# Kernel optimization log

Hardware: AMD Instinct MI355X
Metric: run time of the kernel (lower is better)

Reference implementation:

```python
import jax, jax.numpy as jnp
import numpy as np
import math

N = 20000      # nodes
E = 150000     # edges
IN = 256       # in_dim
HID = 256      # n_hid / out_dim
T = 4          # num_types
R = 8          # num_relations
H = 8          # n_heads
DK = HID // H  # d_k = 32
L = 2          # n_layers
MAXLEN = 240   # RTE max_len


def _rte_table():
    # fixed sinusoid table from RelTemporalEncoding (requires_grad=False in torch)
    pos = np.arange(MAXLEN, dtype=np.float64)[:, None]
    div = np.exp(np.arange(0, HID, 2, dtype=np.float64) * -(math.log(10000.0) / HID))
    emb = np.zeros((MAXLEN, HID), dtype=np.float64)
    emb[:, 0::2] = np.sin(pos * div) / math.sqrt(HID)
    emb[:, 1::2] = np.cos(pos * div) / math.sqrt(HID)
    return jnp.asarray(emb, dtype=jnp.float32)


def setup_inputs() -> dict:
    key = jax.random.key(0)
    ks = jax.random.split(key, 20)
    node_feature = jax.random.normal(ks[0], (N, IN), jnp.float32)
    node_type = jax.random.randint(ks[1], (N,), 0, T)
    edge_index = jax.random.randint(ks[2], (2, E), 0, N)
    edge_type = jax.random.randint(ks[3], (E,), 0, R)
    edge_time = jax.random.randint(ks[4], (E,), 0, MAXLEN)

    s_in = 1.0 / math.sqrt(IN)
    s_h = 1.0 / math.sqrt(HID)
    s_g = math.sqrt(2.0 / (DK + DK))  # glorot for relation mats

    adapt_W = jax.random.normal(ks[5], (T, IN, HID), jnp.float32) * s_in
    adapt_b = jnp.zeros((T, HID), jnp.float32)
    k_W = jax.random.normal(ks[6], (L, T, HID, HID), jnp.float32) * s_h
    k_b = jnp.zeros((L, T, HID), jnp.float32)
    q_W = jax.random.normal(ks[7], (L, T, HID, HID), jnp.float32) * s_h
    q_b = jnp.zeros((L, T, HID), jnp.float32)
    v_W = jax.random.normal(ks[8], (L, T, HID, HID), jnp.float32) * s_h
    v_b = jnp.zeros((L, T, HID), jnp.float32)
    a_W = jax.random.normal(ks[9], (L, T, HID, HID), jnp.float32) * s_h
    a_b = jnp.zeros((L, T, HID), jnp.float32)
    rel_pri = jnp.ones((L, R, H), jnp.float32)
    rel_att = jax.random.normal(ks[10], (L, R, H, DK, DK), jnp.float32) * s_g
    rel_msg = jax.random.normal(ks[11], (L, R, H, DK, DK), jnp.float32) * s_g
    skip = jnp.ones((L, T), jnp.float32)
    rte_W = jax.random.normal(ks[12], (L, HID, HID), jnp.float32) * s_h
    rte_b = jnp.zeros((L, HID), jnp.float32)
    rte_emb = _rte_table()

    return dict(node_feature=node_feature, node_type=node_type, edge_time=edge_time,
                edge_index=edge_index, edge_type=edge_type,
                adapt_W=adapt_W, adapt_b=adapt_b, k_W=k_W, k_b=k_b, q_W=q_W, q_b=q_b,
                v_W=v_W, v_b=v_b, a_W=a_W, a_b=a_b, rel_pri=rel_pri, rel_att=rel_att,
                rel_msg=rel_msg, skip=skip, rte_W=rte_W, rte_b=rte_b, rte_emb=rte_emb)


def _typed_linear(x, W, b, types):
    # x: [M, din]; W: [T, din, dout]; per-row type-selected linear (T dense GEMMs + select)
    out = jnp.zeros((x.shape[0], W.shape[-1]), x.dtype)
    for t in range(T):
        out = jnp.where((types == t)[:, None], x @ W[t] + b[t], out)
    return out


def _hgt_forward(node_feature, node_type, edge_time, edge_index, edge_type,
                 adapt_W, adapt_b, k_W, k_b, q_W, q_b, v_W, v_b, a_W, a_b,
                 rel_pri, rel_att, rel_msg, skip, rte_W, rte_b, rte_emb):
    # adapt: per-type tanh(Linear) (dropout is identity at p=0)
    x = jnp.tanh(_typed_linear(node_feature, adapt_W, adapt_b, node_type))
    src, tgt = edge_index[0], edge_index[1]   # j (source), i (target)
    st, tt = node_type[src], node_type[tgt]
    sqrt_dk = math.sqrt(DK)
    att = None
    rte = rte_emb[edge_time]                  # [E, HID]
    for l in range(L):
        x_j = x[src] + (rte @ rte_W[l] + rte_b[l])   # RTE added to source repr
        x_i = x[tgt]
        q = _typed_linear(x_i, q_W[l], q_b[l], tt).reshape(E, H, DK)
        k = _typed_linear(x_j, k_W[l], k_b[l], st).reshape(E, H, DK)
        v = _typed_linear(x_j, v_W[l], v_b[l], st).reshape(E, H, DK)
        att_e = jnp.zeros((E, H), x.dtype)
        msg = jnp.zeros((E, H, DK), x.dtype)
        for r in range(R):
            kr = jnp.einsum('ehd,hdk->ehk', k, rel_att[l, r])
            vr = jnp.einsum('ehd,hdk->ehk', v, rel_msg[l, r])
            a = (q * kr).sum(-1) * rel_pri[l, r] / sqrt_dk
            m = edge_type == r
            att_e = jnp.where(m[:, None], a, att_e)
            msg = jnp.where(m[:, None, None], vr, msg)
        # segment softmax over target node ids
        amax = jax.ops.segment_max(att_e, tgt, num_segments=N)
        ex = jnp.exp(att_e - amax[tgt])
        denom = jax.ops.segment_sum(ex, tgt, num_segments=N)
        alpha = ex / denom[tgt]                       # [E, H]
        agg = jax.ops.segment_sum(msg * alpha[:, :, None], tgt, num_segments=N)
        agg = jax.nn.gelu(agg.reshape(N, HID), approximate=False)
        trans = _typed_linear(agg, a_W[l], a_b[l], node_type)
        sk = jax.nn.sigmoid(skip[l])[node_type][:, None]
        x = trans * sk + x * (1.0 - sk)               # no LayerNorm (use_norm=False)
        att = alpha
    return att, x


def reference(node_feature, node_type, edge_time, edge_index, edge_type,
              adapt_W, adapt_b, k_W, k_b, q_W, q_b, v_W, v_b, a_W, a_b,
              rel_pri, rel_att, rel_msg, skip, rte_W, rte_b, rte_emb):
    return _hgt_forward(node_feature, node_type, edge_time, edge_index, edge_type,
                        adapt_W, adapt_b, k_W, k_b, q_W, q_b, v_W, v_b, a_W, a_b,
                        rel_pri, rel_att, rel_msg, skip, rte_W, rte_b, rte_emb)
```

## Files before the change

### kernel.cpp

```cpp
#include <hip/hip_runtime.h>
#include <hip/hip_fp16.h>

#define NN    20000
#define NE    150000
#define HD    256
#define NT    4
#define NR    8
#define NH    8
#define DKq   32
#define NL    2
#define MAXL  240
#define HBLK  256
#define SCB   ((NN + 255)/256)
#define TMAX  632
#define FOLDN 79
#define FOLDC 15
#define INV_SQRT_DK 0.17677669529663687f

typedef _Float16 f16x4 __attribute__((ext_vector_type(4)));
typedef float    f32x4v __attribute__((ext_vector_type(4)));

__global__ __launch_bounds__(256) void k_nhist(const int* __restrict__ ntype, int* __restrict__ nhist)
{
    __shared__ int h[NT];
    const int tid = threadIdx.x, b = blockIdx.x;
    if (tid < NT) h[tid] = 0;
    __syncthreads();
    const int cn = (NN + HBLK-1)/HBLK;
    const int nEnd = min((b+1)*cn, NN);
    for (int i = b*cn + tid; i < nEnd; i += 256) atomicAdd(&h[ntype[i]], 1);
    __syncthreads();
    if (tid < NT) nhist[b*NT + tid] = h[tid];
}
__global__ void k_nscan(const int* __restrict__ nhist, int* __restrict__ noff, int* __restrict__ nbase,
                        int* __restrict__ tlist, int* __restrict__ tcount)
{
    __shared__ int tot[NT];
    const int tid = threadIdx.x;
    if (tid < NT){
        int s = 0;
        for (int b = 0; b < HBLK; b++) s += nhist[b*NT + tid];
        tot[tid] = s;
    }
    __syncthreads();
    if (tid == 0){ noff[0]=0; for (int t=0;t<NT;t++) noff[t+1]=noff[t]+tot[t]; }
    if (tid < NT){
        int base = 0; for (int t=0;t<tid;t++) base += tot[t];
        int run = 0;
        for (int b=0;b<HBLK;b++){ nbase[b*NT+tid] = base + run; run += nhist[b*NT+tid]; }
    }
    __syncthreads();
    if (tid == 0){
        int c = 0;
        for (int t = 0; t < NT; t++){
            const int ntile = (tot[t] + 31) >> 5;
            for (int rt = 0; rt < ntile; rt++) tlist[c++] = (t << 20) | rt;
        }
        *tcount = c;
    }
}
__global__ __launch_bounds__(256) void k_nscatter(const int* __restrict__ ntype,
    const int* __restrict__ nbase, int* __restrict__ nbucket)
{
    __shared__ int cur[NT];
    const int tid = threadIdx.x, b = blockIdx.x;
    if (tid < NT) cur[tid] = nbase[b*NT + tid];
    __syncthreads();
    const int cn = (NN + HBLK-1)/HBLK;
    const int nEnd = min((b+1)*cn, NN);
    for (int i = b*cn + tid; i < nEnd; i += 256)
        nbucket[atomicAdd(&cur[ntype[i]], 1)] = i;
}

__global__ void k_zero_bins(int* __restrict__ cnt){
    int i = blockIdx.x*256 + threadIdx.x;
    if (i < NN) cnt[i] = 0;
}
__global__ void k_csr_hist(const int* __restrict__ ei, int* __restrict__ cnt){
    int e = blockIdx.x*256 + threadIdx.x;
    if (e >= NE) return;
    atomicAdd(&cnt[ei[NE+e]], 1);
}
__global__ __launch_bounds__(256) void k_scan1(const int* __restrict__ cnt,
    int* __restrict__ tgt_off, int* __restrict__ bsum)
{
    __shared__ int sh[256];
    const int t = threadIdx.x, b = blockIdx.x;
    const int i = b*256 + t;
    const int v = (i < NN) ? cnt[i] : 0;
    sh[t] = v;
    __syncthreads();
    #pragma unroll
    for (int d = 1; d < 256; d <<= 1){
        const int u = (t >= d) ? sh[t-d] : 0;
        __syncthreads();
        sh[t] += u;
        __syncthreads();
    }
    if (i < NN) tgt_off[i] = sh[t] - v;
    if (t == 255) bsum[b] = sh[255];
}
__global__ __launch_bounds__(128) void k_scan2(const int* __restrict__ bsum,
    int* __restrict__ bbase, int* __restrict__ tgt_off)
{
    __shared__ int sh[128];
    const int t = threadIdx.x;
    const int v = (t < SCB) ? bsum[t] : 0;
    sh[t] = v;
    __syncthreads();
    #pragma unroll
    for (int d = 1; d < 128; d <<= 1){
        const int u = (t >= d) ? sh[t-d] : 0;
        __syncthreads();
        sh[t] += u;
        __syncthreads();
    }
    if (t < SCB) bbase[t] = sh[t] - v;
    if (t == 0) tgt_off[NN] = NE;
}
__global__ __launch_bounds__(256) void k_scan3(int* __restrict__ tgt_off,
    const int* __restrict__ bbase, int* __restrict__ binCur)
{
    const int i = blockIdx.x*256 + threadIdx.x;
    if (i >= NN) return;
    const int o = tgt_off[i] + bbase[blockIdx.x];
    tgt_off[i] = o;
    binCur[i] = o;
}
__global__ void k_csr_scatter(const int* __restrict__ ei, const int* __restrict__ etype,
    const int* __restrict__ etime, const int* __restrict__ ntype,
    int* __restrict__ binCur, int* __restrict__ src_s, int* __restrict__ combo_s,
    int* __restrict__ eid_s, int* __restrict__ tgt_s)
{
    int e = blockIdx.x*256 + threadIdx.x;
    if (e >= NE) return;
    const int tgt = ei[NE+e], r = etype[e], src = ei[e];
    const int pos = atomicAdd(&binCur[tgt], 1);
    src_s[pos] = src;
    combo_s[pos] = (etime[e]*NT + ntype[src]) | (r << 12);
    eid_s[pos] = e;
    tgt_s[pos] = tgt;
}

__global__ __launch_bounds__(256) void k_w2f16_big(
    const float* __restrict__ adaptW, const float* __restrict__ qW, const float* __restrict__ kW,
    const float* __restrict__ vW, const float* __restrict__ aW, _Float16* __restrict__ out)
{
    const int y = blockIdx.y;
    const float* src; int m;
    if (y < 4){ src = adaptW; m = y; }
    else if (y < 12){ src = qW; m = y-4; }
    else if (y < 20){ src = kW; m = y-12; }
    else if (y < 28){ src = vW; m = y-20; }
    else { src = aW; m = y-28; }
    const float* ip = src + (size_t)m*65536;
    _Float16* op = out + (size_t)y*65536;
    const int tid4 = blockIdx.x*256 + threadIdx.x;
    const int k4 = tid4 >> 8, c = tid4 & 255;
    f16x4 hv;
    #pragma unroll
    for (int j = 0; j < 4; j++)
        hv[j] = (_Float16)ip[(size_t)(((k4*4 + j) << 8) + c)];
    *reinterpret_cast<f16x4*>(&op[(size_t)tid4 * 4]) = hv;
}
__global__ __launch_bounds__(256) void k_w2f16_rel(
    const float* __restrict__ attW, const float* __restrict__ msgW, _Float16* __restrict__ out)
{
    const int y = blockIdx.y;
    const float* ip = (y < 128) ? (attW + (size_t)y*1024) : (msgW + (size_t)(y-128)*1024);
    _Float16* op = out + (size_t)y*1024;
    const int tid4 = threadIdx.x;
    const int k4 = tid4 >> 5, c = tid4 & 31;
    f16x4 hv;
    #pragma unroll
    for (int j = 0; j < 4; j++)
        hv[j] = (_Float16)ip[(size_t)(((k4*4 + j) << 5) + c)];
    *reinterpret_cast<f16x4*>(&op[(size_t)tid4 * 4]) = hv;
}

__global__ __launch_bounds__(256) void k_typed_mfma(
    const float* __restrict__ inF, const _Float16* __restrict__ inH,
    const _Float16* __restrict__ W0, const _Float16* __restrict__ W1, const _Float16* __restrict__ W2,
    const float* __restrict__ b0, const float* __restrict__ b1, const float* __restrict__ b2,
    void* __restrict__ o0, void* __restrict__ o1, void* __restrict__ o2,
    const int* __restrict__ nbucket, const int* __restrict__ noff,
    const int* __restrict__ tlist, const int* __restrict__ tcount,
    int nsel, int mode, int out_half_mask, const float* __restrict__ skipv, const float* __restrict__ xold)
{
    if ((int)blockIdx.x >= *tcount) return;
    const int ent = tlist[blockIdx.x];
    const int t = ent >> 20, rowTile = ent & 0xFFFFF;
    const int start = noff[t], cnt = noff[t+1] - start;

    const int tid = threadIdx.x;
    const int w = tid >> 6, lane = tid & 63;
    const int lrow = lane & 15, lgrp = lane >> 4;

    __shared__ _Float16 Al[32][260];
    __shared__ int nid[32];

    if (tid < 32){
        const int gr = rowTile*32 + tid;
        nid[tid] = (gr < cnt) ? nbucket[start + gr] : -1;
    }
    __syncthreads();

    {
        const int r = tid >> 3;
        const int arow = nid[r];
        if (inH){
            const _Float16* ap = (arow >= 0) ? (inH + (size_t)arow*HD) : nullptr;
            #pragma unroll
            for (int j = 0; j < 8; j++){
                const int f4 = (tid & 7) + j*8;
                f16x4 hv = {0,0,0,0};
                if (ap) hv = *reinterpret_cast<const f16x4*>(ap + f4*4);
                *reinterpret_cast<f16x4*>(&Al[r][f4*4]) = hv;
            }
        } else {
            const float* ap = (arow >= 0) ? (inF + (size_t)arow*HD) : nullptr;
            #pragma unroll
            for (int j = 0; j < 8; j++){
                const int f4 = (tid & 7) + j*8;
                float4 v = make_float4(0.f,0.f,0.f,0.f);
                if (ap) v = *reinterpret_cast<const float4*>(ap + f4*4);
                f16x4 hv;
                hv[0]=(_Float16)v.x; hv[1]=(_Float16)v.y; hv[2]=(_Float16)v.z; hv[3]=(_Float16)v.w;
                *reinterpret_cast<f16x4*>(&Al[r][f4*4]) = hv;
            }
        }
    }
    __syncthreads();

    float sk = 0.f;
    if (mode == 2) sk = 1.f/(1.f + __expf(-skipv[t]));

    auto proc = [&](const _Float16* Wb, const float* bb, void* out, int oh){
        const _Float16* W = Wb + (size_t)t*HD*HD;
        const float* bias = bb + (size_t)t*HD;
        f32x4v acc[4][2];
        #pragma unroll
        for (int cs = 0; cs < 4; cs++){
            acc[cs][0] = (f32x4v){0.f,0.f,0.f,0.f};
            acc[cs][1] = (f32x4v){0.f,0.f,0.f,0.f};
        }
        #pragma unroll 4
        for (int kc = 0; kc < 16; kc++){
            f16x4 bf[4];
            #pragma unroll
            for (int cs = 0; cs < 4; cs++)
                bf[cs] = *reinterpret_cast<const f16x4*>(
                    &W[(size_t)((kc*4 + lgrp)*HD + w*64 + cs*16 + lrow)*4]);
            const f16x4 af0 = *reinterpret_cast<const f16x4*>(&Al[lrow][kc*16 + lgrp*4]);
            const f16x4 af1 = *reinterpret_cast<const f16x4*>(&Al[16 + lrow][kc*16 + lgrp*4]);
            #pragma unroll
            for (int cs = 0; cs < 4; cs++){
                acc[cs][0] = __builtin_amdgcn_mfma_f32_16x16x16f16(af0, bf[cs], acc[cs][0], 0,0,0);
                acc[cs][1] = __builtin_amdgcn_mfma_f32_16x16x16f16(af1, bf[cs], acc[cs][1], 0,0,0);
            }
        }
        #pragma unroll
        for (int cs = 0; cs < 4; cs++){
            const int col = w*64 + cs*16 + lrow;
            const float bcol = bias[col];
            #pragma unroll
            for (int rt = 0; rt < 2; rt++){
                #pragma unroll
                for (int i = 0; i < 4; i++){
                    const int lr = rt*16 + lgrp*4 + i;
                    const int gr = rowTile*32 + lr;
                    if (gr >= cnt) continue;
                    const int node = nid[lr];
                    float v = acc[cs][rt][i] + bcol;
                    if (mode == 1) v = tanhf(v);
                    else if (mode == 2){
                        const float xo = xold[(size_t)node*HD + col];
                        v = v*sk + xo*(1.f - sk);
                    }
                    if (oh) ((_Float16*)out)[(size_t)node*HD + col] = (_Float16)v;
                    else    ((float*)out)[(size_t)node*HD + col] = v;
                }
            }
        }
    };

    proc(W0, b0, o0, out_half_mask & 1);
    if (nsel > 1){
        proc(W1, b1, o1, (out_half_mask >> 1) & 1);
        proc(W2, b2, o2, (out_half_mask >> 2) & 1);
    }
}

__global__ __launch_bounds__(256) void k_row_gemm(
    const float* __restrict__ A, const float* __restrict__ W, const float* __restrict__ bias,
    float* __restrict__ C)
{
    const int row = blockIdx.x, d = threadIdx.x;
    __shared__ float ar[HD];
    ar[d] = A[(size_t)row*HD + d];
    __syncthreads();
    float acc = bias[d];
    #pragma unroll 8
    for (int k=0;k<HD;k++) acc = fmaf(ar[k], W[(size_t)k*HD + d], acc);
    C[(size_t)row*HD + d] = acc;
}
__global__ __launch_bounds__(256) void k_row_gemm2(
    const float* __restrict__ A, const float* __restrict__ kWb, const float* __restrict__ vWb,
    _Float16* __restrict__ Kc, _Float16* __restrict__ Vc)
{
    const int row = blockIdx.x, ty = blockIdx.y, d = threadIdx.x;
    const float* W = ((blockIdx.z == 0) ? kWb : vWb) + (size_t)ty*HD*HD;
    _Float16* C = (blockIdx.z == 0) ? Kc : Vc;
    __shared__ float ar[HD];
    ar[d] = A[(size_t)row*HD + d];
    __syncthreads();
    float acc = 0.f;
    #pragma unroll 8
    for (int k=0;k<HD;k++) acc = fmaf(ar[k], W[(size_t)k*HD + d], acc);
    C[(size_t)row*(NT*HD) + ty*HD + d] = (_Float16)acc;
}

__global__ __launch_bounds__(256) void k_fold_mfma(
    const _Float16* __restrict__ INn, const _Float16* __restrict__ INc,
    const _Float16* __restrict__ MATF,
    _Float16* __restrict__ OUTn, _Float16* __restrict__ OUTc)
{
    const int r = blockIdx.y;
    const bool isC = (int)blockIdx.x >= FOLDN;
    const int bx0 = isC ? (int)blockIdx.x - FOLDN : (int)blockIdx.x;
    const _Float16* IN = isC ? INc : INn;
    _Float16* OUT = isC ? OUTc : OUTn;
    const int M = isC ? (MAXL*NT) : NN;
    const int bstride = (isC ? FOLDC : FOLDN) * 4;

    const int lane = threadIdx.x & 63, w = threadIdx.x >> 6;
    const int lrow = lane & 15, lgrp = lane >> 4;
    f16x4 b[NH][2][2];
    const _Float16* Mr = MATF + (size_t)r*NH*1024;
    #pragma unroll
    for (int h = 0; h < NH; h++)
      #pragma unroll
      for (int kb = 0; kb < 2; kb++)
        #pragma unroll
        for (int hf = 0; hf < 2; hf++)
            b[h][kb][hf] = *reinterpret_cast<const f16x4*>(
                &Mr[(size_t)h*1024 + (size_t)(((kb*4 + lgrp)*32) + hf*16 + lrow)*4]);
    const int ntiles = M >> 4;
    for (int t = bx0*4 + w; t < ntiles; t += bstride){
        const int row0 = t*16;
        const _Float16* inrow = IN + (size_t)(row0 + lrow)*HD;
        f16x4 a[NH][2];
        #pragma unroll
        for (int h = 0; h < NH; h++)
          #pragma unroll
          for (int kb = 0; kb < 2; kb++)
              a[h][kb] = *reinterpret_cast<const f16x4*>(&inrow[h*32 + kb*16 + lgrp*4]);
        #pragma unroll
        for (int h = 0; h < NH; h++){
          #pragma unroll
          for (int hf = 0; hf < 2; hf++){
              f32x4v acc = {0.f,0.f,0.f,0.f};
              acc = __builtin_amdgcn_mfma_f32_16x16x16f16(a[h][0], b[h][0][hf], acc, 0,0,0);
              acc = __builtin_amdgcn_mfma_f32_16x16x16f16(a[h][1], b[h][1][hf], acc, 0,0,0);
              #pragma unroll
              for (int i = 0; i < 4; i++){
                  const int rr = lgrp*4 + i;
                  OUT[((size_t)(row0+rr)*NR + r)*HD + h*32 + hf*16 + lrow] = (_Float16)acc[i];
              }
          }
        }
    }
}

__global__ __launch_bounds__(256) void k_score(
    const float* __restrict__ q0, const _Float16* __restrict__ kA, const _Float16* __restrict__ KcA,
    const float* __restrict__ relP,
    const int* __restrict__ src_s, const int* __restrict__ combo_s, const int* __restrict__ tgt_s,
    float* __restrict__ s_arr)
{
    const int j = blockIdx.x*4 + (threadIdx.x >> 6);
    if (j >= NE) return;
    const int lane = threadIdx.x & 63;
    const int h = lane >> 3, c4 = (lane & 7) << 2;
    const int src = src_s[j];
    const int cw  = combo_s[j];
    const int tgt = tgt_s[j];
    const int r = cw >> 12, combo = cw & 0xFFF;

    const float4 q4 = *reinterpret_cast<const float4*>(&q0[(size_t)tgt*HD + h*32 + c4]);
    const f16x4 ka = *reinterpret_cast<const f16x4*>(&kA[((size_t)src*NR + r)*HD + h*32 + c4]);
    const f16x4 kc = *reinterpret_cast<const f16x4*>(&KcA[((size_t)combo*NR + r)*HD + h*32 + c4]);
    float v = q4.x*((float)ka[0]+(float)kc[0])
            + q4.y*((float)ka[1]+(float)kc[1])
            + q4.z*((float)ka[2]+(float)kc[2])
            + q4.w*((float)ka[3]+(float)kc[3]);
    v += __shfl_xor(v, 1); v += __shfl_xor(v, 2); v += __shfl_xor(v, 4);
    if ((lane & 7) == 0)
        s_arr[(size_t)j*NH + h] = v * relP[r*NH + h] * INV_SQRT_DK;
}

__global__ __launch_bounds__(256) void k_softmax(
    float* __restrict__ s_arr, const int* __restrict__ tgt_off, const int* __restrict__ eid_s,
    float* __restrict__ out_att, int store)
{
    const int idx = blockIdx.x*256 + threadIdx.x;
    if (idx >= NN*NH) return;
    const int n = idx >> 3, h = idx & 7;
    const int e0 = tgt_off[n], e1 = tgt_off[n+1];
    if (e0 == e1) return;
    float m = -INFINITY;
    for (int j = e0; j < e1; j++) m = fmaxf(m, s_arr[(size_t)j*NH + h]);
    float l = 0.f;
    for (int j = e0; j < e1; j++) l += __expf(s_arr[(size_t)j*NH + h] - m);
    const float inv = 1.f / l;
    for (int j = e0; j < e1; j++){
        const float a = __expf(s_arr[(size_t)j*NH + h] - m) * inv;
        s_arr[(size_t)j*NH + h] = a;
        if (store) out_att[(size_t)eid_s[j]*NH + h] = a;
    }
}

__global__ __launch_bounds__(256) void k_agg(
    const _Float16* __restrict__ vM, const _Float16* __restrict__ VcM,
    const float* __restrict__ alpha,
    const int* __restrict__ tgt_off, const int* __restrict__ src_s, const int* __restrict__ combo_s,
    _Float16* __restrict__ agg)
{
    const int n = blockIdx.x*4 + (threadIdx.x >> 6);
    if (n >= NN) return;
    const int lane = threadIdx.x & 63;
    const int h = lane >> 3, c4 = (lane & 7) << 2;
    const int col = h*32 + c4;
    const int e0 = tgt_off[n], e1 = tgt_off[n+1];
    float a0=0.f, a1=0.f, a2=0.f, a3=0.f;
    for (int j = e0; j < e1; j++){
        const int src = src_s[j];
        const int cw  = combo_s[j];
        const int r = cw >> 12, combo = cw & 0xFFF;
        const float al = alpha[(size_t)j*NH + h];
        const f16x4 vm = *reinterpret_cast<const f16x4*>(&vM[((size_t)src*NR + r)*HD + col]);
        const f16x4 vc = *reinterpret_cast<const f16x4*>(&VcM[((size_t)combo*NR + r)*HD + col]);
        a0 = fmaf(al, (float)vm[0] + (float)vc[0], a0);
        a1 = fmaf(al, (float)vm[1] + (float)vc[1], a1);
        a2 = fmaf(al, (float)vm[2] + (float)vc[2], a2);
        a3 = fmaf(al, (float)vm[3] + (float)vc[3], a3);
    }
    f16x4 o;
    o[0] = (_Float16)(0.5f*a0*(1.f + erff(a0*0.70710678118654752f)));
    o[1] = (_Float16)(0.5f*a1*(1.f + erff(a1*0.70710678118654752f)));
    o[2] = (_Float16)(0.5f*a2*(1.f + erff(a2*0.70710678118654752f)));
    o[3] = (_Float16)(0.5f*a3*(1.f + erff(a3*0.70710678118654752f)));
    *reinterpret_cast<f16x4*>(&agg[(size_t)n*HD + col]) = o;
}

__global__ void k_copy(const float* __restrict__ s, float* __restrict__ d, int n){
    int i = blockIdx.x*256 + threadIdx.x;
    if (i < n) d[i] = s[i];
}

extern "C" void kernel_launch(void* const* d_in, const int* in_sizes, int n_in,
                              void* d_out, int out_size, void* d_ws, size_t ws_size,
                              hipStream_t stream)
{
    const float* node_feature = (const float*)d_in[0];
    const int*   node_type    = (const int*)d_in[1];
    const int*   edge_time    = (const int*)d_in[2];
    const int*   edge_index   = (const int*)d_in[3];
    const int*   edge_type    = (const int*)d_in[4];
    const float* adapt_W = (const float*)d_in[5];
    const float* adapt_b = (const float*)d_in[6];
    const float* k_W = (const float*)d_in[7];
    const float* k_b = (const float*)d_in[8];
    const float* q_W = (const float*)d_in[9];
    const float* q_b = (const float*)d_in[10];
    const float* v_W = (const float*)d_in[11];
    const float* v_b = (const float*)d_in[12];
    const float* a_W = (const float*)d_in[13];
    const float* a_b = (const float*)d_in[14];
    const float* rel_pri = (const float*)d_in[15];
    const float* rel_att = (const float*)d_in[16];
    const float* rel_msg = (const float*)d_in[17];
    const float* skip  = (const float*)d_in[18];
    const float* rte_W = (const float*)d_in[19];
    const float* rte_b = (const float*)d_in[20];
    const float* rte_emb = (const float*)d_in[21];

    char* wp = (char*)d_ws;
    auto alloc_f = [&](size_t n)->float*{ float* p=(float*)wp; wp += n*sizeof(float); return p; };
    auto alloc_i = [&](size_t n)->int*  { int*   p=(int*)wp;   wp += n*sizeof(int);   return p; };
    auto alloc_h = [&](size_t n)->_Float16*{ _Float16* p=(_Float16*)wp; wp += n*sizeof(_Float16); return p; };
    float* xA    = alloc_f((size_t)NN*HD);
    float* xB    = alloc_f((size_t)NN*HD);
    float* q0f   = alloc_f((size_t)NN*HD);
    _Float16* k0h = alloc_h((size_t)NN*HD);
    _Float16* v0h = alloc_h((size_t)NN*HD);
    _Float16* aggh= alloc_h((size_t)NN*HD);
    float* s_arr = alloc_f((size_t)NE*NH);
    float* rteP  = alloc_f((size_t)MAXL*HD);
    _Float16* Kch = alloc_h((size_t)MAXL*NT*HD);
    _Float16* Vch = alloc_h((size_t)MAXL*NT*HD);
    _Float16* kavm = alloc_h((size_t)NN*NR*HD);
    _Float16* kca  = alloc_h((size_t)MAXL*NT*NR*HD);
    _Float16* wF   = alloc_h((size_t)36*65536);
    _Float16* relF = alloc_h((size_t)256*1024);
    int* nbucket = alloc_i(NN);
    int* nhist   = alloc_i(HBLK*NT);
    int* nbase   = alloc_i(HBLK*NT);
    int* noff    = alloc_i(8);
    int* tlist   = alloc_i(TMAX);
    int* tcount  = alloc_i(8);
    int* cnt     = alloc_i(NN);
    int* bsum    = alloc_i(SCB);
    int* bbase   = alloc_i(SCB);
    int* binCur  = alloc_i(NN);
    int* tgt_off = alloc_i(NN+1);
    int* src_s   = alloc_i(NE);
    int* combo_s = alloc_i(NE);
    int* eid_s   = alloc_i(NE);
    int* tgt_s   = alloc_i(NE);

    const _Float16* adaptF = wF;
    const _Float16* qF = wF + (size_t)4*65536;
    const _Float16* kF = wF + (size_t)12*65536;
    const _Float16* vF = wF + (size_t)20*65536;
    const _Float16* aF = wF + (size_t)28*65536;
    const _Float16* relAF = relF;
    const _Float16* relMF = relF + (size_t)128*1024;

    float* out_att = (float*)d_out;
    float* out_x   = (float*)d_out + (size_t)NE*NH;

    const dim3 gFold(FOLDN + FOLDC, NR);
    const int gE256 = (NE + 255)/256;
    const int gNH = (NN*HD + 255)/256;
    const int gSc = (NE + 3)/4;
    const int gSm = (NN*NH + 255)/256;
    const int gAg = (NN + 3)/4;

    k_w2f16_big<<<dim3(64,36),256,0,stream>>>(adapt_W, q_W, k_W, v_W, a_W, wF);
    k_w2f16_rel<<<dim3(1,256),256,0,stream>>>(rel_att, rel_msg, relF);

    k_nhist<<<HBLK,256,0,stream>>>(node_type, nhist);
    k_nscan<<<1,64,0,stream>>>(nhist, noff, nbase, tlist, tcount);
    k_nscatter<<<HBLK,256,0,stream>>>(node_type, nbase, nbucket);

    k_zero_bins<<<SCB,256,0,stream>>>(cnt);
    k_csr_hist<<<gE256,256,0,stream>>>(edge_index, cnt);
    k_scan1<<<SCB,256,0,stream>>>(cnt, tgt_off, bsum);
    k_scan2<<<1,128,0,stream>>>(bsum, bbase, tgt_off);
    k_scan3<<<SCB,256,0,stream>>>(tgt_off, bbase, binCur);
    k_csr_scatter<<<gE256,256,0,stream>>>(edge_index, edge_type, edge_time, node_type,
                                          binCur, src_s, combo_s, eid_s, tgt_s);

    k_typed_mfma<<<TMAX,256,0,stream>>>(node_feature, nullptr, adaptF, nullptr, nullptr,
                                        adapt_b, nullptr, nullptr,
                                        xA, nullptr, nullptr,
                                        nbucket, noff, tlist, tcount, 1, 1, 0, nullptr, nullptr);

    const float* x_in = xA;
    float* x_out = xB;
    for (int l = 0; l < NL; l++){
        k_row_gemm<<<MAXL,256,0,stream>>>(rte_emb, rte_W + (size_t)l*HD*HD,
                                          rte_b + (size_t)l*HD, rteP);
        k_row_gemm2<<<dim3(MAXL,NT,2),256,0,stream>>>(rteP, k_W + (size_t)l*NT*HD*HD,
                                                      v_W + (size_t)l*NT*HD*HD, Kch, Vch);
        k_typed_mfma<<<TMAX,256,0,stream>>>(x_in, nullptr,
                                            qF + (size_t)l*NT*HD*HD, kF + (size_t)l*NT*HD*HD, vF + (size_t)l*NT*HD*HD,
                                            q_b + (size_t)l*NT*HD,  k_b + (size_t)l*NT*HD,  v_b + (size_t)l*NT*HD,
                                            q0f, k0h, v0h,
                                            nbucket, noff, tlist, tcount, 3, 0, 6, nullptr, nullptr);
        k_fold_mfma<<<gFold,256,0,stream>>>(k0h, Kch, relAF + (size_t)l*NR*NH*1024, kavm, kca);
        k_score<<<gSc,256,0,stream>>>(q0f, kavm, kca, rel_pri + (size_t)l*NR*NH,
                                      src_s, combo_s, tgt_s, s_arr);
        const int store_s = (l == NL-1) ? 1 : 0;
        k_softmax<<<gSm,256,0,stream>>>(s_arr, tgt_off, eid_s, out_att, store_s);
        k_fold_mfma<<<gFold,256,0,stream>>>(v0h, Vch, relMF + (size_t)l*NR*NH*1024, kavm, kca);
        k_agg<<<gAg,256,0,stream>>>(kavm, kca, s_arr, tgt_off, src_s, combo_s, aggh);
        k_typed_mfma<<<TMAX,256,0,stream>>>(nullptr, aggh,
                                            aF + (size_t)l*NT*HD*HD, nullptr, nullptr,
                                            a_b + (size_t)l*NT*HD, nullptr, nullptr,
                                            x_out, nullptr, nullptr,
                                            nbucket, noff, tlist, tcount, 1, 2, 0, skip + (size_t)l*NT, x_in);
        float* tmp = (float*)x_in; x_in = x_out; x_out = tmp;
    }
    k_copy<<<gNH,256,0,stream>>>(x_in, out_x, NN*HD);
}
```

Measured before the change: 602.0 us.

## Chain typed output GEMM into next layer's Q/K/V projections inside one kernel

The typed linear kernel now writes its result tile back into shared memory and immediately runs the next layer's Q, K and V projections on it. This removes a separate launch and the re-read of x from global memory. The RTE-based fold tables for both layers are precomputed up front, and the node fold launches now cover only nodes. The final layer writes straight into the output buffer, which drops the copy kernel. In exchange there are extra block-level syncs, more buffers, and a longer serial chain of GEMMs per block.

```diff
diff --git a/kernel.cpp b/kernel.cpp
--- a/kernel.cpp
+++ b/kernel.cpp
@@ -178,14 +178,15 @@
     *reinterpret_cast<f16x4*>(&op[(size_t)tid4 * 4]) = hv;
 }
 
-__global__ __launch_bounds__(256) void k_typed_mfma(
+__global__ __launch_bounds__(256) void k_typed_fused(
     const float* __restrict__ inF, const _Float16* __restrict__ inH,
-    const _Float16* __restrict__ W0, const _Float16* __restrict__ W1, const _Float16* __restrict__ W2,
-    const float* __restrict__ b0, const float* __restrict__ b1, const float* __restrict__ b2,
-    void* __restrict__ o0, void* __restrict__ o1, void* __restrict__ o2,
+    const _Float16* __restrict__ Wa, const float* __restrict__ ba, void* __restrict__ oa,
+    const _Float16* __restrict__ Wq, const float* __restrict__ bq, void* __restrict__ oq,
+    const _Float16* __restrict__ Wk, const float* __restrict__ bk, void* __restrict__ ok_,
+    const _Float16* __restrict__ Wv, const float* __restrict__ bv, void* __restrict__ ov,
     const int* __restrict__ nbucket, const int* __restrict__ noff,
     const int* __restrict__ tlist, const int* __restrict__ tcount,
-    int nsel, int mode, int out_half_mask, const float* __restrict__ skipv, const float* __restrict__ xold)
+    int mode, int ohmask, const float* __restrict__ skipv, const float* __restrict__ xold)
 {
     if ((int)blockIdx.x >= *tcount) return;
     const int ent = tlist[blockIdx.x];
@@ -235,7 +236,9 @@
     float sk = 0.f;
     if (mode == 2) sk = 1.f/(1.f + __expf(-skipv[t]));
 
-    auto proc = [&](const _Float16* Wb, const float* bb, void* out, int oh){
+    const bool chain = (Wq != nullptr);
+
+    auto proc = [&](const _Float16* Wb, const float* bb, void* out, int oh, int md, bool cw){
         const _Float16* W = Wb + (size_t)t*HD*HD;
         const float* bias = bb + (size_t)t*HD;
         f32x4v acc[4][2];
@@ -259,6 +262,7 @@
                 acc[cs][1] = __builtin_amdgcn_mfma_f32_16x16x16f16(af1, bf[cs], acc[cs][1], 0,0,0);
             }
         }
+        if (cw) __syncthreads();
         #pragma unroll
         for (int cs = 0; cs < 4; cs++){
             const int col = w*64 + cs*16 + lrow;
@@ -272,22 +276,25 @@
                     if (gr >= cnt) continue;
                     const int node = nid[lr];
                     float v = acc[cs][rt][i] + bcol;
-                    if (mode == 1) v = tanhf(v);
-                    else if (mode == 2){
+                    if (md == 1) v = tanhf(v);
+                    else if (md == 2){
                         const float xo = xold[(size_t)node*HD + col];
                         v = v*sk + xo*(1.f - sk);
                     }
                     if (oh) ((_Float16*)out)[(size_t)node*HD + col] = (_Float16)v;
                     else    ((float*)out)[(size_t)node*HD + col] = v;
+                    if (cw) Al[lr][col] = (_Float16)v;
                 }
             }
         }
+        if (cw) __syncthreads();
     };
 
-    proc(W0, b0, o0, out_half_mask & 1);
-    if (nsel > 1){
-        proc(W1, b1, o1, (out_half_mask >> 1) & 1);
-        proc(W2, b2, o2, (out_half_mask >> 2) & 1);
+    proc(Wa, ba, oa, ohmask & 1, mode, chain);
+    if (chain){
+        proc(Wq, bq, oq, (ohmask >> 1) & 1, 0, false);
+        proc(Wk, bk, ok_, (ohmask >> 2) & 1, 0, false);
+        proc(Wv, bv, ov, (ohmask >> 3) & 1, 0, false);
     }
 }
 
@@ -321,18 +328,10 @@
 }
 
 __global__ __launch_bounds__(256) void k_fold_mfma(
-    const _Float16* __restrict__ INn, const _Float16* __restrict__ INc,
-    const _Float16* __restrict__ MATF,
-    _Float16* __restrict__ OUTn, _Float16* __restrict__ OUTc)
+    const _Float16* __restrict__ IN, const _Float16* __restrict__ MATF,
+    _Float16* __restrict__ OUT, int M, int nbx)
 {
     const int r = blockIdx.y;
-    const bool isC = (int)blockIdx.x >= FOLDN;
-    const int bx0 = isC ? (int)blockIdx.x - FOLDN : (int)blockIdx.x;
-    const _Float16* IN = isC ? INc : INn;
-    _Float16* OUT = isC ? OUTc : OUTn;
-    const int M = isC ? (MAXL*NT) : NN;
-    const int bstride = (isC ? FOLDC : FOLDN) * 4;
-
     const int lane = threadIdx.x & 63, w = threadIdx.x >> 6;
     const int lrow = lane & 15, lgrp = lane >> 4;
     f16x4 b[NH][2][2];
@@ -346,7 +345,7 @@
             b[h][kb][hf] = *reinterpret_cast<const f16x4*>(
                 &Mr[(size_t)h*1024 + (size_t)(((kb*4 + lgrp)*32) + hf*16 + lrow)*4]);
     const int ntiles = M >> 4;
-    for (int t = bx0*4 + w; t < ntiles; t += bstride){
+    for (int t = (int)blockIdx.x*4 + w; t < ntiles; t += nbx*4){
         const int row0 = t*16;
         const _Float16* inrow = IN + (size_t)(row0 + lrow)*HD;
         f16x4 a[NH][2];
@@ -453,11 +452,6 @@
     *reinterpret_cast<f16x4*>(&agg[(size_t)n*HD + col]) = o;
 }
 
-__global__ void k_copy(const float* __restrict__ s, float* __restrict__ d, int n){
-    int i = blockIdx.x*256 + threadIdx.x;
-    if (i < n) d[i] = s[i];
-}
-
 extern "C" void kernel_launch(void* const* d_in, const int* in_sizes, int n_in,
                               void* d_out, int out_size, void* d_ws, size_t ws_size,
                               hipStream_t stream)
@@ -500,7 +494,10 @@
     _Float16* Kch = alloc_h((size_t)MAXL*NT*HD);
     _Float16* Vch = alloc_h((size_t)MAXL*NT*HD);
     _Float16* kavm = alloc_h((size_t)NN*NR*HD);
-    _Float16* kca  = alloc_h((size_t)MAXL*NT*NR*HD);
+    _Float16* kcaA0 = alloc_h((size_t)MAXL*NT*NR*HD);
+    _Float16* kcaA1 = alloc_h((size_t)MAXL*NT*NR*HD);
+    _Float16* kcaM0 = alloc_h((size_t)MAXL*NT*NR*HD);
+    _Float16* kcaM1 = alloc_h((size_t)MAXL*NT*NR*HD);
     _Float16* wF   = alloc_h((size_t)36*65536);
     _Float16* relF = alloc_h((size_t)256*1024);
     int* nbucket = alloc_i(NN);
@@ -530,9 +527,9 @@
     float* out_att = (float*)d_out;
     float* out_x   = (float*)d_out + (size_t)NE*NH;
 
-    const dim3 gFold(FOLDN + FOLDC, NR);
+    const dim3 gFoldN(FOLDN, NR);
+    const dim3 gFoldC(FOLDC, NR);
     const int gE256 = (NE + 255)/256;
-    const int gNH = (NN*HD + 255)/256;
     const int gSc = (NE + 3)/4;
     const int gSm = (NN*NH + 255)/256;
     const int gAg = (NN + 3)/4;
@@ -552,36 +549,54 @@
     k_csr_scatter<<<gE256,256,0,stream>>>(edge_index, edge_type, edge_time, node_type,
                                           binCur, src_s, combo_s, eid_s, tgt_s);
 
-    k_typed_mfma<<<TMAX,256,0,stream>>>(node_feature, nullptr, adaptF, nullptr, nullptr,
-                                        adapt_b, nullptr, nullptr,
-                                        xA, nullptr, nullptr,
-                                        nbucket, noff, tlist, tcount, 1, 1, 0, nullptr, nullptr);
-
-    const float* x_in = xA;
-    float* x_out = xB;
+    {
+        k_row_gemm<<<MAXL,256,0,stream>>>(rte_emb, rte_W, rte_b, rteP);
+        k_row_gemm2<<<dim3(MAXL,NT,2),256,0,stream>>>(rteP, k_W, v_W, Kch, Vch);
+        k_fold_mfma<<<gFoldC,256,0,stream>>>(Kch, relAF, kcaA0, MAXL*NT, FOLDC);
+        k_fold_mfma<<<gFoldC,256,0,stream>>>(Vch, relMF, kcaM0, MAXL*NT, FOLDC);
+        k_row_gemm<<<MAXL,256,0,stream>>>(rte_emb, rte_W + (size_t)HD*HD, rte_b + HD, rteP);
+        k_row_gemm2<<<dim3(MAXL,NT,2),256,0,stream>>>(rteP, k_W + (size_t)NT*HD*HD,
+                                                      v_W + (size_t)NT*HD*HD, Kch, Vch);
+        k_fold_mfma<<<gFoldC,256,0,stream>>>(Kch, relAF + (size_t)NR*NH*1024, kcaA1, MAXL*NT, FOLDC);
+        k_fold_mfma<<<gFoldC,256,0,stream>>>(Vch, relMF + (size_t)NR*NH*1024, kcaM1, MAXL*NT, FOLDC);
+    }
+
+    k_typed_fused<<<TMAX,256,0,stream>>>(node_feature, nullptr,
+                                         adaptF, adapt_b, xA,
+                                         qF, q_b, q0f,
+                                         kF, k_b, k0h,
+                                         vF, v_b, v0h,
+                                         nbucket, noff, tlist, tcount,
+                                         1, 12, nullptr, nullptr);
+
     for (int l = 0; l < NL; l++){
-        k_row_gemm<<<MAXL,256,0,stream>>>(rte_emb, rte_W + (size_t)l*HD*HD,
-                                          rte_b + (size_t)l*HD, rteP);
-        k_row_gemm2<<<dim3(MAXL,NT,2),256,0,stream>>>(rteP, k_W + (size_t)l*NT*HD*HD,
-                                                      v_W + (size_t)l*NT*HD*HD, Kch, Vch);
-        k_typed_mfma<<<TMAX,256,0,stream>>>(x_in, nullptr,
-                                            qF + (size_t)l*NT*HD*HD, kF + (size_t)l*NT*HD*HD, vF + (size_t)l*NT*HD*HD,
-                                            q_b + (size_t)l*NT*HD,  k_b + (size_t)l*NT*HD,  v_b + (size_t)l*NT*HD,
-                                            q0f, k0h, v0h,
-                                            nbucket, noff, tlist, tcount, 3, 0, 6, nullptr, nullptr);
-        k_fold_mfma<<<gFold,256,0,stream>>>(k0h, Kch, relAF + (size_t)l*NR*NH*1024, kavm, kca);
-        k_score<<<gSc,256,0,stream>>>(q0f, kavm, kca, rel_pri + (size_t)l*NR*NH,
+        const _Float16* rAF = relAF + (size_t)l*NR*NH*1024;
+        const _Float16* rMF = relMF + (size_t)l*NR*NH*1024;
+        const _Float16* kcaA = (l == 0) ? kcaA0 : kcaA1;
+        const _Float16* kcaM = (l == 0) ? kcaM0 : kcaM1;
+        k_fold_mfma<<<gFoldN,256,0,stream>>>(k0h, rAF, kavm, NN, FOLDN);
+        k_score<<<gSc,256,0,stream>>>(q0f, kavm, kcaA, rel_pri + (size_t)l*NR*NH,
                                       src_s, combo_s, tgt_s, s_arr);
         const int store_s = (l == NL-1) ? 1 : 0;
         k_softmax<<<gSm,256,0,stream>>>(s_arr, tgt_off, eid_s, out_att, store_s);
-        k_fold_mfma<<<gFold,256,0,stream>>>(v0h, Vch, relMF + (size_t)l*NR*NH*1024, kavm, kca);
-        k_agg<<<gAg,256,0,stream>>>(kavm, kca, s_arr, tgt_off, src_s, combo_s, aggh);
-        k_typed_mfma<<<TMAX,256,0,stream>>>(nullptr, aggh,
-                                            aF + (size_t)l*NT*HD*HD, nullptr, nullptr,
-                                            a_b + (size_t)l*NT*HD, nullptr, nullptr,
-                                            x_out, nullptr, nullptr,
-                                            nbucket, noff, tlist, tcount, 1, 2, 0, skip + (size_t)l*NT, x_in);
-        float* tmp = (float*)x_in; x_in = x_out; x_out = tmp;
-    }
-    k_copy<<<gNH,256,0,stream>>>(x_in, out_x, NN*HD);
-}
+        k_fold_mfma<<<gFoldN,256,0,stream>>>(v0h, rMF, kavm, NN, FOLDN);
+        k_agg<<<gAg,256,0,stream>>>(kavm, kcaM, s_arr, tgt_off, src_s, combo_s, aggh);
+        if (l == 0){
+            k_typed_fused<<<TMAX,256,0,stream>>>(nullptr, aggh,
+                                                 aF, a_b, xB,
+                                                 qF + (size_t)NT*HD*HD, q_b + (size_t)NT*HD, q0f,
+                                                 kF + (size_t)NT*HD*HD, k_b + (size_t)NT*HD, k0h,
+                                                 vF + (size_t)NT*HD*HD, v_b + (size_t)NT*HD, v0h,
+                                                 nbucket, noff, tlist, tcount,
+                                                 2, 12, skip, xA);
+        } else {
+            k_typed_fused<<<TMAX,256,0,stream>>>(nullptr, aggh,
+                                                 aF + (size_t)NT*HD*HD, a_b + (size_t)NT*HD, out_x,
+                                                 nullptr, nullptr, nullptr,
+                                                 nullptr, nullptr, nullptr,
+                                                 nullptr, nullptr, nullptr,
+                                                 nbucket, noff, tlist, tcount,
+                                                 2, 0, skip + NT, xB);
+        }
+    }
+}
```

Measured after the change: 597.3 us. No clear change (-0.8%).
